# Performance work log

Hardware: AMD Instinct MI355X
Metric: run time of the kernel (lower is better)

Reference implementation:

```python
import jax, jax.numpy as jnp
import numpy as np

EPS = 1e-6

def elu_feature_map(x):
    return jax.nn.elu(x) + 1.0

def setup_inputs() -> dict:
    key = jax.random.key(0)
    kq, kk, kv = jax.random.split(key, 3)
    N, L, S, H, D = 8, 8192, 8192, 8, 32
    return {
        "queries": jax.random.normal(kq, (N, L, H, D), dtype=jnp.float32),
        "keys": jax.random.normal(kk, (N, S, H, D), dtype=jnp.float32),
        "values": jax.random.normal(kv, (N, S, H, D), dtype=jnp.float32),
    }

def reference(queries, keys, values):
    # Linear (kernelized) attention, default path of MixAttention.forward
    Q = elu_feature_map(queries)            # [N,L,H,D]
    K = elu_feature_map(keys)               # [N,S,H,D]
    v_length = values.shape[1]
    vals = values / v_length                # [N,S,H,D]
    KV = jnp.einsum('nshd,nshv->nhdv', K, vals)          # [N,H,D,D]
    Z = 1.0 / (jnp.einsum('nlhd,nhd->nlh', Q, K.sum(axis=1)) + EPS)  # [N,L,H]
    out = jnp.einsum('nlhd,nhdv,nlh->nlhv', Q, KV, Z) * v_length     # [N,L,H,D]
    return out
```

## Files before the change

kernel.cpp:

```cpp
#include <hip/hip_runtime.h>


constexpr int N_ = 8, L_ = 8192, S_ = 8192, H_ = 8, D_ = 32;
constexpr int NH = N_ * H_;
constexpr int PART_STRIDE = D_ * D_ + D_;
constexpr int LCH = 256;
constexpr float EPS_ = 1e-6f;
constexpr int HD = H_ * D_;
constexpr int CHUNK = 16;

__device__ __forceinline__ float fmap(float x) {
    return x > 0.0f ? x + 1.0f : __expf(x);
}

template<int SPL>
__global__ __launch_bounds__(512, 8) void lin_attn_phase1(
        const float* __restrict__ Kg, const float* __restrict__ Vg,
        float* __restrict__ part) {
    constexpr int CS_BLK = S_ / SPL;
    constexpr int ROUNDS = CS_BLK / CHUNK;
    const int n  = blockIdx.x / SPL;
    const int sc = blockIdx.x % SPL;
    const int t = threadIdx.x;
    const int w = t >> 6;
    const int i = t & 63;
    const int c4 = i << 2;
    const int d0 = (i >> 3) << 2;
    const int v0 = (i & 7) << 2;
    const int hcol = w * D_;

    __shared__ __align__(16) float Kt[CHUNK][HD];
    __shared__ __align__(16) float Vt[CHUNK][HD];

    float acc[4][4];
    #pragma unroll
    for (int a = 0; a < 4; ++a)
        #pragma unroll
        for (int b = 0; b < 4; ++b) acc[a][b] = 0.0f;
    float kp[4] = {0.f, 0.f, 0.f, 0.f};

    const float* Kbase = Kg + (size_t)n * S_ * HD + (size_t)sc * CS_BLK * HD;
    const float* Vbase = Vg + (size_t)n * S_ * HD + (size_t)sc * CS_BLK * HD;

    #pragma unroll 1
    for (int r = 0; r < ROUNDS; ++r) {
        const float* ks = Kbase + (size_t)r * CHUNK * HD;
        const float* vs = Vbase + (size_t)r * CHUNK * HD;
        float4 k0 = *reinterpret_cast<const float4*>(ks + (size_t)w * HD + c4);
        float4 k1 = *reinterpret_cast<const float4*>(ks + (size_t)(w + 8) * HD + c4);
        const float4 u0 = *reinterpret_cast<const float4*>(vs + (size_t)w * HD + c4);
        const float4 u1 = *reinterpret_cast<const float4*>(vs + (size_t)(w + 8) * HD + c4);
        k0.x = fmap(k0.x); k0.y = fmap(k0.y); k0.z = fmap(k0.z); k0.w = fmap(k0.w);
        k1.x = fmap(k1.x); k1.y = fmap(k1.y); k1.z = fmap(k1.z); k1.w = fmap(k1.w);
        kp[0] += k0.x + k1.x; kp[1] += k0.y + k1.y;
        kp[2] += k0.z + k1.z; kp[3] += k0.w + k1.w;
        __syncthreads();
        *reinterpret_cast<float4*>(&Kt[w][c4])     = k0;
        *reinterpret_cast<float4*>(&Kt[w + 8][c4]) = k1;
        *reinterpret_cast<float4*>(&Vt[w][c4])     = u0;
        *reinterpret_cast<float4*>(&Vt[w + 8][c4]) = u1;
        __syncthreads();
        #pragma unroll
        for (int s = 0; s < CHUNK; ++s) {
            const float4 ka = *reinterpret_cast<const float4*>(&Kt[s][hcol + d0]);
            const float4 vq = *reinterpret_cast<const float4*>(&Vt[s][hcol + v0]);
            const float kd[4] = {ka.x, ka.y, ka.z, ka.w};
            const float vv[4] = {vq.x, vq.y, vq.z, vq.w};
            #pragma unroll
            for (int a = 0; a < 4; ++a)
                #pragma unroll
                for (int b = 0; b < 4; ++b)
                    acc[a][b] += kd[a] * vv[b];
        }
    }

    float* P = part + ((size_t)sc * NH + n * H_ + w) * PART_STRIDE;
    #pragma unroll
    for (int a = 0; a < 4; ++a)
        *reinterpret_cast<float4*>(&P[(d0 + a) * D_ + v0]) =
            make_float4(acc[a][0], acc[a][1], acc[a][2], acc[a][3]);

    __syncthreads();
    float* ksl = &Kt[0][0];
    *reinterpret_cast<float4*>(&ksl[w * HD + c4]) =
        make_float4(kp[0], kp[1], kp[2], kp[3]);
    __syncthreads();
    if (t < 64) {
        float4 s4 = make_float4(0.f, 0.f, 0.f, 0.f);
        #pragma unroll
        for (int g = 0; g < 8; ++g) {
            const float4 rr = *reinterpret_cast<const float4*>(&ksl[g * HD + (t << 2)]);
            s4.x += rr.x; s4.y += rr.y; s4.z += rr.z; s4.w += rr.w;
        }
        float* P2 = part + ((size_t)sc * NH + n * H_ + (t >> 3)) * PART_STRIDE;
        *reinterpret_cast<float4*>(&P2[D_ * D_ + ((t & 7) << 2)]) = s4;
    }
}

template<int SPL>
__global__ __launch_bounds__(256) void lin_attn_reduce(
        const float* __restrict__ part, float* __restrict__ red) {
    const int i = blockIdx.x * 256 + threadIdx.x;
    if (i >= NH * PART_STRIDE) return;
    float s = 0.0f;
    #pragma unroll 16
    for (int sc = 0; sc < SPL; ++sc)
        s += part[(size_t)sc * (NH * PART_STRIDE) + i];
    red[i] = s;
}

__global__ __launch_bounds__(256) void lin_attn_phase2(
        const float* __restrict__ Qg, const float* __restrict__ red,
        float* __restrict__ outg) {
    constexpr int QTS = 32;
    constexpr int NLC = L_ / LCH;
    const int nh  = blockIdx.x / NLC;
    const int lcb = blockIdx.x % NLC;
    const int n = nh / H_, h = nh % H_;
    const int t = threadIdx.x;
    const int v  = t & 31;
    const int rb = t >> 5;
    const int r  = t >> 3;
    const int c  = (t & 7) << 2;

    __shared__ __align__(16) float Qt[QTS][D_];
    __shared__ float zinv_sh[QTS];

    float kv[D_];
    const float* W = red + (size_t)nh * PART_STRIDE;
    #pragma unroll
    for (int d = 0; d < D_; ++d) kv[d] = W[d * D_ + v];
    const float4 ksq = *reinterpret_cast<const float4*>(W + D_ * D_ + c);

    const size_t base = (size_t)n * L_ * H_ * D_ + (size_t)h * D_;
    const int l0 = lcb * LCH;
    for (int step = 0; step < LCH; step += QTS) {
        const float4 q4 = *reinterpret_cast<const float4*>(
            Qg + base + (size_t)(l0 + step + r) * (H_ * D_) + c);
        __syncthreads();
        float4 qf;
        qf.x = fmap(q4.x); qf.y = fmap(q4.y);
        qf.z = fmap(q4.z); qf.w = fmap(q4.w);
        *reinterpret_cast<float4*>(&Qt[r][c]) = qf;
        float zp = qf.x * ksq.x + qf.y * ksq.y + qf.z * ksq.z + qf.w * ksq.w;
        zp += __shfl_xor(zp, 1);
        zp += __shfl_xor(zp, 2);
        zp += __shfl_xor(zp, 4);
        if ((t & 7) == 0) zinv_sh[r] = 1.0f / (zp + EPS_);
        __syncthreads();
        #pragma unroll
        for (int rr = 0; rr < 4; ++rr) {
            const int row = (rr << 3) + rb;
            float acc = 0.0f;
            #pragma unroll
            for (int d2 = 0; d2 < 16; ++d2) {
                const float2 q = *reinterpret_cast<const float2*>(&Qt[row][d2 << 1]);
                acc += q.x * kv[(d2 << 1)] + q.y * kv[(d2 << 1) + 1];
            }
            outg[base + (size_t)(l0 + step + row) * (H_ * D_) + v] =
                acc * zinv_sh[row];
        }
    }
}

extern "C" void kernel_launch(void* const* d_in, const int* in_sizes, int n_in,
                              void* d_out, int out_size, void* d_ws, size_t ws_size,
                              hipStream_t stream) {
    const float* Q = (const float*)d_in[0];
    const float* K = (const float*)d_in[1];
    const float* V = (const float*)d_in[2];
    float* out  = (float*)d_out;
    float* part = (float*)d_ws;

    const size_t need128 = ((size_t)128 + 1) * NH * PART_STRIDE * sizeof(float);
    if (ws_size >= need128) {
        constexpr int SP = 128;
        float* red = part + (size_t)SP * NH * PART_STRIDE;
        lin_attn_phase1<SP><<<N_ * SP, 512, 0, stream>>>(K, V, part);
        lin_attn_reduce<SP><<<(NH * PART_STRIDE + 255) / 256, 256, 0, stream>>>(part, red);
        lin_attn_phase2<<<NH * (L_ / LCH), 256, 0, stream>>>(Q, red, out);
    } else {
        constexpr int SP = 64;
        float* red = part + (size_t)SP * NH * PART_STRIDE;
        lin_attn_phase1<SP><<<N_ * SP, 512, 0, stream>>>(K, V, part);
        lin_attn_reduce<SP><<<(NH * PART_STRIDE + 255) / 256, 256, 0, stream>>>(part, red);
        lin_attn_phase2<<<NH * (L_ / LCH), 256, 0, stream>>>(Q, red, out);
    }
}
```

Measured before the change: 86.39 us.

## Prefetch next K/V chunk into registers and give each thread an 8x4 KV tile

Phase 1 now runs 256 threads per block. Each thread computes an 8x4 block of the KV outer-product accumulator instead of 4x4, which doubles register work per shared-memory read. The global loads for the next chunk are issued before the compute loop of the current chunk, giving register double-buffering that hides memory latency. The chunk size drops to 8 rows, so there are more rounds and more barriers, and register pressure rises with fewer threads per block.

```diff
diff --git a/kernel.cpp b/kernel.cpp
--- a/kernel.cpp
+++ b/kernel.cpp
@@ -7,14 +7,14 @@
 constexpr int LCH = 256;
 constexpr float EPS_ = 1e-6f;
 constexpr int HD = H_ * D_;
-constexpr int CHUNK = 16;
+constexpr int CHUNK = 8;
 
 __device__ __forceinline__ float fmap(float x) {
     return x > 0.0f ? x + 1.0f : __expf(x);
 }
 
 template<int SPL>
-__global__ __launch_bounds__(512, 8) void lin_attn_phase1(
+__global__ __launch_bounds__(256, 4) void lin_attn_phase1(
         const float* __restrict__ Kg, const float* __restrict__ Vg,
         float* __restrict__ part) {
     constexpr int CS_BLK = S_ / SPL;
@@ -22,73 +22,85 @@
     const int n  = blockIdx.x / SPL;
     const int sc = blockIdx.x % SPL;
     const int t = threadIdx.x;
-    const int w = t >> 6;
-    const int i = t & 63;
-    const int c4 = i << 2;
-    const int d0 = (i >> 3) << 2;
+    const int hg = t >> 5;
+    const int i  = t & 31;
+    const int d0 = (i >> 3) << 3;
     const int v0 = (i & 7) << 2;
-    const int hcol = w * D_;
+    const int hcol = hg * D_;
+    const int cc = (t & 63) << 2;
 
     __shared__ __align__(16) float Kt[CHUNK][HD];
     __shared__ __align__(16) float Vt[CHUNK][HD];
 
-    float acc[4][4];
+    float acc[8][4];
     #pragma unroll
-    for (int a = 0; a < 4; ++a)
+    for (int a = 0; a < 8; ++a)
         #pragma unroll
         for (int b = 0; b < 4; ++b) acc[a][b] = 0.0f;
     float kp[4] = {0.f, 0.f, 0.f, 0.f};
 
-    const float* Kbase = Kg + (size_t)n * S_ * HD + (size_t)sc * CS_BLK * HD;
-    const float* Vbase = Vg + (size_t)n * S_ * HD + (size_t)sc * CS_BLK * HD;
+    const float* Kb = Kg + (size_t)n * S_ * HD + (size_t)sc * CS_BLK * HD;
+    const float* Vb = Vg + (size_t)n * S_ * HD + (size_t)sc * CS_BLK * HD;
+    const int t4 = t << 2;
+
+    float4 ka = *reinterpret_cast<const float4*>(Kb + t4);
+    float4 kb = *reinterpret_cast<const float4*>(Kb + t4 + 1024);
+    float4 ua = *reinterpret_cast<const float4*>(Vb + t4);
+    float4 ub = *reinterpret_cast<const float4*>(Vb + t4 + 1024);
 
     #pragma unroll 1
     for (int r = 0; r < ROUNDS; ++r) {
-        const float* ks = Kbase + (size_t)r * CHUNK * HD;
-        const float* vs = Vbase + (size_t)r * CHUNK * HD;
-        float4 k0 = *reinterpret_cast<const float4*>(ks + (size_t)w * HD + c4);
-        float4 k1 = *reinterpret_cast<const float4*>(ks + (size_t)(w + 8) * HD + c4);
-        const float4 u0 = *reinterpret_cast<const float4*>(vs + (size_t)w * HD + c4);
-        const float4 u1 = *reinterpret_cast<const float4*>(vs + (size_t)(w + 8) * HD + c4);
-        k0.x = fmap(k0.x); k0.y = fmap(k0.y); k0.z = fmap(k0.z); k0.w = fmap(k0.w);
-        k1.x = fmap(k1.x); k1.y = fmap(k1.y); k1.z = fmap(k1.z); k1.w = fmap(k1.w);
-        kp[0] += k0.x + k1.x; kp[1] += k0.y + k1.y;
-        kp[2] += k0.z + k1.z; kp[3] += k0.w + k1.w;
-        __syncthreads();
-        *reinterpret_cast<float4*>(&Kt[w][c4])     = k0;
-        *reinterpret_cast<float4*>(&Kt[w + 8][c4]) = k1;
-        *reinterpret_cast<float4*>(&Vt[w][c4])     = u0;
-        *reinterpret_cast<float4*>(&Vt[w + 8][c4]) = u1;
-        __syncthreads();
+        __syncthreads();
+        float4 kaf, kbf;
+        kaf.x = fmap(ka.x); kaf.y = fmap(ka.y);
+        kaf.z = fmap(ka.z); kaf.w = fmap(ka.w);
+        kbf.x = fmap(kb.x); kbf.y = fmap(kb.y);
+        kbf.z = fmap(kb.z); kbf.w = fmap(kb.w);
+        kp[0] += kaf.x + kbf.x; kp[1] += kaf.y + kbf.y;
+        kp[2] += kaf.z + kbf.z; kp[3] += kaf.w + kbf.w;
+        *reinterpret_cast<float4*>(&Kt[0][0] + t4)        = kaf;
+        *reinterpret_cast<float4*>(&Kt[0][0] + t4 + 1024) = kbf;
+        *reinterpret_cast<float4*>(&Vt[0][0] + t4)        = ua;
+        *reinterpret_cast<float4*>(&Vt[0][0] + t4 + 1024) = ub;
+        __syncthreads();
+        if (r + 1 < ROUNDS) {
+            const float* ks = Kb + (size_t)(r + 1) * CHUNK * HD;
+            const float* vs = Vb + (size_t)(r + 1) * CHUNK * HD;
+            ka = *reinterpret_cast<const float4*>(ks + t4);
+            kb = *reinterpret_cast<const float4*>(ks + t4 + 1024);
+            ua = *reinterpret_cast<const float4*>(vs + t4);
+            ub = *reinterpret_cast<const float4*>(vs + t4 + 1024);
+        }
         #pragma unroll
         for (int s = 0; s < CHUNK; ++s) {
-            const float4 ka = *reinterpret_cast<const float4*>(&Kt[s][hcol + d0]);
+            const float4 k1 = *reinterpret_cast<const float4*>(&Kt[s][hcol + d0]);
+            const float4 k2 = *reinterpret_cast<const float4*>(&Kt[s][hcol + d0 + 4]);
             const float4 vq = *reinterpret_cast<const float4*>(&Vt[s][hcol + v0]);
-            const float kd[4] = {ka.x, ka.y, ka.z, ka.w};
+            const float kd[8] = {k1.x, k1.y, k1.z, k1.w, k2.x, k2.y, k2.z, k2.w};
             const float vv[4] = {vq.x, vq.y, vq.z, vq.w};
             #pragma unroll
-            for (int a = 0; a < 4; ++a)
+            for (int a = 0; a < 8; ++a)
                 #pragma unroll
                 for (int b = 0; b < 4; ++b)
                     acc[a][b] += kd[a] * vv[b];
         }
     }
 
-    float* P = part + ((size_t)sc * NH + n * H_ + w) * PART_STRIDE;
+    float* P = part + ((size_t)sc * NH + n * H_ + hg) * PART_STRIDE;
     #pragma unroll
-    for (int a = 0; a < 4; ++a)
+    for (int a = 0; a < 8; ++a)
         *reinterpret_cast<float4*>(&P[(d0 + a) * D_ + v0]) =
             make_float4(acc[a][0], acc[a][1], acc[a][2], acc[a][3]);
 
     __syncthreads();
     float* ksl = &Kt[0][0];
-    *reinterpret_cast<float4*>(&ksl[w * HD + c4]) =
+    *reinterpret_cast<float4*>(&ksl[(t >> 6) * HD + cc]) =
         make_float4(kp[0], kp[1], kp[2], kp[3]);
     __syncthreads();
     if (t < 64) {
         float4 s4 = make_float4(0.f, 0.f, 0.f, 0.f);
         #pragma unroll
-        for (int g = 0; g < 8; ++g) {
+        for (int g = 0; g < 4; ++g) {
             const float4 rr = *reinterpret_cast<const float4*>(&ksl[g * HD + (t << 2)]);
             s4.x += rr.x; s4.y += rr.y; s4.z += rr.z; s4.w += rr.w;
         }
@@ -176,13 +188,13 @@
     if (ws_size >= need128) {
         constexpr int SP = 128;
         float* red = part + (size_t)SP * NH * PART_STRIDE;
-        lin_attn_phase1<SP><<<N_ * SP, 512, 0, stream>>>(K, V, part);
+        lin_attn_phase1<SP><<<N_ * SP, 256, 0, stream>>>(K, V, part);
         lin_attn_reduce<SP><<<(NH * PART_STRIDE + 255) / 256, 256, 0, stream>>>(part, red);
         lin_attn_phase2<<<NH * (L_ / LCH), 256, 0, stream>>>(Q, red, out);
     } else {
         constexpr int SP = 64;
         float* red = part + (size_t)SP * NH * PART_STRIDE;
-        lin_attn_phase1<SP><<<N_ * SP, 512, 0, stream>>>(K, V, part);
+        lin_attn_phase1<SP><<<N_ * SP, 256, 0, stream>>>(K, V, part);
         lin_attn_reduce<SP><<<(NH * PART_STRIDE + 255) / 256, 256, 0, stream>>>(part, red);
         lin_attn_phase2<<<NH * (L_ / LCH), 256, 0, stream>>>(Q, red, out);
     }
```

Result: slower. 100.8 us (+16.7%).

## Restructure KV accumulation to per-thread 4x32 tiles with wave-local V exchange

Applied to the files above, without the earlier changes.

Phase 1 now uses 256-thread blocks. Each thread accumulates a 4x32 slice of K^T V for its own row and head, instead of staging 16-row chunks of K and V in shared memory behind two block barriers per round. V rows are shared within a wave through a small swizzled LDS buffer with no block-wide sync, and K/V loads are register double-buffered so global fetches overlap compute. Partials from the 4 waves are reduced through LDS at the end. The 128 accumulator registers per thread will lower occupancy, and the wave-local LDS exchange has no explicit barrier.

```diff
diff --git a/kernel.cpp b/kernel.cpp
--- a/kernel.cpp
+++ b/kernel.cpp
@@ -7,93 +7,120 @@
 constexpr int LCH = 256;
 constexpr float EPS_ = 1e-6f;
 constexpr int HD = H_ * D_;
-constexpr int CHUNK = 16;
 
 __device__ __forceinline__ float fmap(float x) {
     return x > 0.0f ? x + 1.0f : __expf(x);
 }
 
 template<int SPL>
-__global__ __launch_bounds__(512, 8) void lin_attn_phase1(
+__global__ __launch_bounds__(256, 2) void lin_attn_phase1(
         const float* __restrict__ Kg, const float* __restrict__ Vg,
         float* __restrict__ part) {
     constexpr int CS_BLK = S_ / SPL;
-    constexpr int ROUNDS = CS_BLK / CHUNK;
+    constexpr int BEATS = CS_BLK / 4;
     const int n  = blockIdx.x / SPL;
     const int sc = blockIdx.x % SPL;
     const int t = threadIdx.x;
     const int w = t >> 6;
-    const int i = t & 63;
-    const int c4 = i << 2;
-    const int d0 = (i >> 3) << 2;
-    const int v0 = (i & 7) << 2;
-    const int hcol = w * D_;
-
-    __shared__ __align__(16) float Kt[CHUNK][HD];
-    __shared__ __align__(16) float Vt[CHUNK][HD];
-
-    float acc[4][4];
+    const int l = t & 63;
+    const int g = l >> 3;
+    const int q = l & 7;
+
+    __shared__ __align__(16) float4 vbuf[4][2][64];
+    __shared__ __align__(16) float red4[4][64][36];
+
+    float acc[4][32];
     #pragma unroll
     for (int a = 0; a < 4; ++a)
         #pragma unroll
-        for (int b = 0; b < 4; ++b) acc[a][b] = 0.0f;
+        for (int c = 0; c < 32; ++c) acc[a][c] = 0.0f;
     float kp[4] = {0.f, 0.f, 0.f, 0.f};
 
-    const float* Kbase = Kg + (size_t)n * S_ * HD + (size_t)sc * CS_BLK * HD;
-    const float* Vbase = Vg + (size_t)n * S_ * HD + (size_t)sc * CS_BLK * HD;
+    const size_t base = (size_t)n * S_ * HD
+                      + (size_t)(sc * CS_BLK + w) * HD + (l << 2);
+    const float* kr = Kg + base;
+    const float* vr = Vg + base;
+    const int wr_slot = (l & ~7) | (q ^ g);
+
+#define PROC(kq_, vq_, par) do {                                               \
+        float kd[4];                                                           \
+        kd[0] = fmap((kq_).x); kd[1] = fmap((kq_).y);                          \
+        kd[2] = fmap((kq_).z); kd[3] = fmap((kq_).w);                          \
+        kp[0] += kd[0]; kp[1] += kd[1]; kp[2] += kd[2]; kp[3] += kd[3];        \
+        vbuf[w][par][wr_slot] = (vq_);                                         \
+        _Pragma("unroll")                                                      \
+        for (int qp = 0; qp < 8; ++qp) {                                       \
+            const float4 vv = vbuf[w][par][(l & ~7) | (qp ^ g)];               \
+            _Pragma("unroll")                                                  \
+            for (int a = 0; a < 4; ++a) {                                      \
+                acc[a][qp * 4 + 0] += kd[a] * vv.x;                            \
+                acc[a][qp * 4 + 1] += kd[a] * vv.y;                            \
+                acc[a][qp * 4 + 2] += kd[a] * vv.z;                            \
+                acc[a][qp * 4 + 3] += kd[a] * vv.w;                            \
+            }                                                                  \
+        }                                                                      \
+    } while (0)
+
+    float4 kA = *reinterpret_cast<const float4*>(kr);
+    float4 vA = *reinterpret_cast<const float4*>(vr);
+    kr += 4 * HD; vr += 4 * HD;
+    float4 kB = *reinterpret_cast<const float4*>(kr);
+    float4 vB = *reinterpret_cast<const float4*>(vr);
+    kr += 4 * HD; vr += 4 * HD;
 
     #pragma unroll 1
-    for (int r = 0; r < ROUNDS; ++r) {
-        const float* ks = Kbase + (size_t)r * CHUNK * HD;
-        const float* vs = Vbase + (size_t)r * CHUNK * HD;
-        float4 k0 = *reinterpret_cast<const float4*>(ks + (size_t)w * HD + c4);
-        float4 k1 = *reinterpret_cast<const float4*>(ks + (size_t)(w + 8) * HD + c4);
-        const float4 u0 = *reinterpret_cast<const float4*>(vs + (size_t)w * HD + c4);
-        const float4 u1 = *reinterpret_cast<const float4*>(vs + (size_t)(w + 8) * HD + c4);
-        k0.x = fmap(k0.x); k0.y = fmap(k0.y); k0.z = fmap(k0.z); k0.w = fmap(k0.w);
-        k1.x = fmap(k1.x); k1.y = fmap(k1.y); k1.z = fmap(k1.z); k1.w = fmap(k1.w);
-        kp[0] += k0.x + k1.x; kp[1] += k0.y + k1.y;
-        kp[2] += k0.z + k1.z; kp[3] += k0.w + k1.w;
-        __syncthreads();
-        *reinterpret_cast<float4*>(&Kt[w][c4])     = k0;
-        *reinterpret_cast<float4*>(&Kt[w + 8][c4]) = k1;
-        *reinterpret_cast<float4*>(&Vt[w][c4])     = u0;
-        *reinterpret_cast<float4*>(&Vt[w + 8][c4]) = u1;
-        __syncthreads();
-        #pragma unroll
-        for (int s = 0; s < CHUNK; ++s) {
-            const float4 ka = *reinterpret_cast<const float4*>(&Kt[s][hcol + d0]);
-            const float4 vq = *reinterpret_cast<const float4*>(&Vt[s][hcol + v0]);
-            const float kd[4] = {ka.x, ka.y, ka.z, ka.w};
-            const float vv[4] = {vq.x, vq.y, vq.z, vq.w};
-            #pragma unroll
-            for (int a = 0; a < 4; ++a)
-                #pragma unroll
-                for (int b = 0; b < 4; ++b)
-                    acc[a][b] += kd[a] * vv[b];
+    for (int i = 0; i < (BEATS - 2) / 2; ++i) {
+        PROC(kA, vA, 0);
+        kA = *reinterpret_cast<const float4*>(kr);
+        vA = *reinterpret_cast<const float4*>(vr);
+        kr += 4 * HD; vr += 4 * HD;
+        PROC(kB, vB, 1);
+        kB = *reinterpret_cast<const float4*>(kr);
+        vB = *reinterpret_cast<const float4*>(vr);
+        kr += 4 * HD; vr += 4 * HD;
+    }
+    PROC(kA, vA, 0);
+    PROC(kB, vB, 1);
+#undef PROC
+
+    const int l2 = t & 63, cb = (t >> 6) * 8;
+    #pragma unroll 1
+    for (int a = 0; a < 4; ++a) {
+        __syncthreads();
+        #pragma unroll
+        for (int c4 = 0; c4 < 8; ++c4)
+            *reinterpret_cast<float4*>(&red4[w][l][c4 * 4]) =
+                make_float4(acc[a][c4 * 4], acc[a][c4 * 4 + 1],
+                            acc[a][c4 * 4 + 2], acc[a][c4 * 4 + 3]);
+        __syncthreads();
+        float4 s0 = make_float4(0.f, 0.f, 0.f, 0.f);
+        float4 s1 = make_float4(0.f, 0.f, 0.f, 0.f);
+        #pragma unroll
+        for (int w2 = 0; w2 < 4; ++w2) {
+            const float4 r0 = *reinterpret_cast<const float4*>(&red4[w2][l2][cb]);
+            const float4 r1 = *reinterpret_cast<const float4*>(&red4[w2][l2][cb + 4]);
+            s0.x += r0.x; s0.y += r0.y; s0.z += r0.z; s0.w += r0.w;
+            s1.x += r1.x; s1.y += r1.y; s1.z += r1.z; s1.w += r1.w;
         }
-    }
-
-    float* P = part + ((size_t)sc * NH + n * H_ + w) * PART_STRIDE;
-    #pragma unroll
-    for (int a = 0; a < 4; ++a)
-        *reinterpret_cast<float4*>(&P[(d0 + a) * D_ + v0]) =
-            make_float4(acc[a][0], acc[a][1], acc[a][2], acc[a][3]);
-
+        float* P = part + ((size_t)sc * NH + n * H_ + (l2 >> 3)) * PART_STRIDE
+                 + (4 * (l2 & 7) + a) * D_ + cb;
+        *reinterpret_cast<float4*>(P)     = s0;
+        *reinterpret_cast<float4*>(P + 4) = s1;
+    }
     __syncthreads();
-    float* ksl = &Kt[0][0];
-    *reinterpret_cast<float4*>(&ksl[w * HD + c4]) =
+    *reinterpret_cast<float4*>(&red4[w][l][0]) =
         make_float4(kp[0], kp[1], kp[2], kp[3]);
     __syncthreads();
     if (t < 64) {
-        float4 s4 = make_float4(0.f, 0.f, 0.f, 0.f);
-        #pragma unroll
-        for (int g = 0; g < 8; ++g) {
-            const float4 rr = *reinterpret_cast<const float4*>(&ksl[g * HD + (t << 2)]);
-            s4.x += rr.x; s4.y += rr.y; s4.z += rr.z; s4.w += rr.w;
+        float4 s = make_float4(0.f, 0.f, 0.f, 0.f);
+        #pragma unroll
+        for (int w2 = 0; w2 < 4; ++w2) {
+            const float4 r = *reinterpret_cast<const float4*>(&red4[w2][t][0]);
+            s.x += r.x; s.y += r.y; s.z += r.z; s.w += r.w;
         }
-        float* P2 = part + ((size_t)sc * NH + n * H_ + (t >> 3)) * PART_STRIDE;
-        *reinterpret_cast<float4*>(&P2[D_ * D_ + ((t & 7) << 2)]) = s4;
+        float* P2 = part + ((size_t)sc * NH + n * H_ + (t >> 3)) * PART_STRIDE
+                  + D_ * D_ + ((t & 7) << 2);
+        *reinterpret_cast<float4*>(P2) = s;
     }
 }
 
@@ -176,13 +203,13 @@
     if (ws_size >= need128) {
         constexpr int SP = 128;
         float* red = part + (size_t)SP * NH * PART_STRIDE;
-        lin_attn_phase1<SP><<<N_ * SP, 512, 0, stream>>>(K, V, part);
+        lin_attn_phase1<SP><<<N_ * SP, 256, 0, stream>>>(K, V, part);
         lin_attn_reduce<SP><<<(NH * PART_STRIDE + 255) / 256, 256, 0, stream>>>(part, red);
         lin_attn_phase2<<<NH * (L_ / LCH), 256, 0, stream>>>(Q, red, out);
     } else {
         constexpr int SP = 64;
         float* red = part + (size_t)SP * NH * PART_STRIDE;
-        lin_attn_phase1<SP><<<N_ * SP, 512, 0, stream>>>(K, V, part);
+        lin_attn_phase1<SP><<<N_ * SP, 256, 0, stream>>>(K, V, part);
         lin_attn_reduce<SP><<<(NH * PART_STRIDE + 255) / 256, 256, 0, stream>>>(part, red);
         lin_attn_phase2<<<NH * (L_ / LCH), 256, 0, stream>>>(Q, red, out);
     }
```

New measurement: 174.9 us. +102.5%, slower.
